# Optimization experiments

Hardware: AMD Instinct MI355X
Metric: run time of the kernel (lower is better)

## Reference

```python
import jax, jax.numpy as jnp
import numpy as np

B, N = 1, 512
CS, CZ, H, CH, PQ, PV = 384, 128, 12, 16, 4, 8
INF, EPS = 1e5, 1e-8
SOFTPLUS_INV_1 = 0.541324854612918


def _init_linear(key, fan_in, fan_out):
    kw, kb = jax.random.split(key)
    std = float(1.0 / np.sqrt(fan_in))
    w = jax.random.normal(kw, (fan_in, fan_out), dtype=jnp.float32) * std
    b = jnp.zeros((fan_out,), dtype=jnp.float32)
    return w, b


def setup_inputs() -> dict:
    key = jax.random.key(0)
    ks = jax.random.split(key, 12)
    s = jax.random.normal(ks[0], (B, N, CS), dtype=jnp.float32)
    z = jax.random.normal(ks[1], (B, N, N, CZ), dtype=jnp.float32) * 0.1
    # proper rotation matrices via QR of random Gaussians
    rot, _ = jnp.linalg.qr(jax.random.normal(ks[2], (B, N, 3, 3), dtype=jnp.float32))
    trans = jax.random.normal(ks[3], (B, N, 3), dtype=jnp.float32) * 10.0
    mask = jnp.ones((B, N), dtype=jnp.float32)
    w_q, b_q = _init_linear(ks[4], CS, H * CH)
    w_kv, b_kv = _init_linear(ks[5], CS, 2 * H * CH)
    w_qp, b_qp = _init_linear(ks[6], CS, H * PQ * 3)
    w_kvp, b_kvp = _init_linear(ks[7], CS, H * (PQ + PV) * 3)
    w_b, b_b = _init_linear(ks[8], CZ, H)
    head_weights = jnp.full((H,), SOFTPLUS_INV_1, dtype=jnp.float32)
    concat_dim = H * (CZ + CH + PV * 4)
    # 'final' init -> zeros
    w_out = jnp.zeros((concat_dim, CS), dtype=jnp.float32)
    b_out = jnp.zeros((CS,), dtype=jnp.float32)
    return dict(s=s, z=z, rot=rot, trans=trans, mask=mask,
                w_q=w_q, b_q=b_q, w_kv=w_kv, b_kv=b_kv,
                w_qp=w_qp, b_qp=b_qp, w_kvp=w_kvp, b_kvp=b_kvp,
                w_b=w_b, b_b=b_b, head_weights=head_weights,
                w_out=w_out, b_out=b_out)


def reference(s, z, rot, trans, mask,
              w_q, b_q, w_kv, b_kv, w_qp, b_qp, w_kvp, b_kvp,
              w_b, b_b, head_weights, w_out, b_out):
    # scalar q/k/v: [B,N,H,CH]
    q = (s @ w_q + b_q).reshape(B, N, H, CH)
    kv = (s @ w_kv + b_kv).reshape(B, N, H, 2 * CH)
    k, v = kv[..., :CH], kv[..., CH:]

    def make_points(w, b, P):
        p = s @ w + b                                   # [B,N,3*H*P] (x|y|z chunks)
        p = jnp.moveaxis(p.reshape(B, N, 3, H * P), -2, -1)  # [B,N,H*P,3]
        p = jnp.einsum('bnij,bnpj->bnpi', rot, p) + trans[:, :, None]  # global frame
        return p.reshape(B, N, H, P, 3)

    q_pts = make_points(w_qp, b_qp, PQ)                 # [B,N,H,PQ,3]
    kv_pts = make_points(w_kvp, b_kvp, PQ + PV)
    k_pts, v_pts = kv_pts[..., :PQ, :], kv_pts[..., PQ:, :]

    # scalar QK attention + pair bias
    a = jnp.einsum('bqhc,bkhc->bhqk', q, k) * float(np.sqrt(1.0 / (3 * CH)))
    b_bias = z @ w_b + b_b                              # [B,N,N,H]
    a = a + float(np.sqrt(1.0 / 3.0)) * jnp.moveaxis(b_bias, -1, -3)

    # squared point-distance attention
    d = q_pts[:, :, None] - k_pts[:, None]              # [B,N,N,H,PQ,3]
    pt_att = jnp.sum(d * d, axis=-1)                    # [B,N,N,H,PQ]
    hw = jax.nn.softplus(head_weights) * float(np.sqrt(1.0 / (3 * (PQ * 9.0 / 2))))
    pt_att = -0.5 * jnp.sum(pt_att * hw[None, None, None, :, None], axis=-1)  # [B,N,N,H]
    a = a + jnp.moveaxis(pt_att, -1, -3)                # [B,H,N,N]

    sq_mask = (mask[:, :, None] * mask[:, None, :] - 1.0) * INF
    a = jax.nn.softmax(a + sq_mask[:, None], axis=-1)   # [B,H,N,N]

    # standard value path
    o = jnp.einsum('bhqk,bkhc->bqhc', a, v).reshape(B, N, H * CH)
    # point value path, rotated back to local frame
    o_pt = jnp.einsum('bhqk,bkhpc->bqhpc', a, v_pts)    # [B,N,H,PV,3]
    o_pt = jnp.einsum('bnji,bnhpj->bnhpi', rot, o_pt - trans[:, :, None, None])
    o_pt_norm = jnp.sqrt(jnp.sum(o_pt ** 2, axis=-1) + EPS).reshape(B, N, H * PV)
    o_pt = o_pt.reshape(B, N, H * PV, 3)
    # pair-weighted path
    o_pair = jnp.einsum('bhqk,bqkc->bqhc', a, z).reshape(B, N, H * CZ)

    o_cat = jnp.concatenate(
        [o, o_pt[..., 0], o_pt[..., 1], o_pt[..., 2], o_pt_norm, o_pair], axis=-1)
    return o_cat @ w_out + b_out
```

## Files before the change

### kernel.cpp

```cpp
#include <hip/hip_runtime.h>
#include <math.h>

#define NRES 512
#define CSD  384
#define CZD  128

#define OFF_Q     0
#define OFF_KT    98304
#define OFF_VC    196608
#define OFF_QP    458752
#define OFF_KPT   532480
#define OFF_A     606208
#define OFF_OCAT  3751936
#define OFF_WCAT  4833280
#define OFF_BCAT  (OFF_WCAT + 442368)
#define OFF_PRAWQ 5276800
#define OFF_PRAWK 5350528
#define OFF_PART  OFF_A

__global__ __launch_bounds__(256) void k_wcat(
    const float* __restrict__ w_q, const float* __restrict__ b_q,
    const float* __restrict__ w_kv, const float* __restrict__ b_kv,
    const float* __restrict__ w_qp, const float* __restrict__ b_qp,
    const float* __restrict__ w_kvp, const float* __restrict__ b_kvp,
    float* __restrict__ wcat, float* __restrict__ bcat)
{
    const int idx = blockIdx.x * 256 + threadIdx.x;
    if (idx < 442368) {
        const int k = idx / 1152, c = idx % 1152;
        float v;
        if (c < 192)      v = w_q[k*192 + c];
        else if (c < 576) v = w_kv[k*384 + (c - 192)];
        else if (c < 720) v = w_qp[k*144 + (c - 576)];
        else              v = w_kvp[k*432 + (c - 720)];
        wcat[idx] = v;
    } else if (idx < 443520) {
        const int c = idx - 442368;
        float v;
        if (c < 192)      v = b_q[c];
        else if (c < 576) v = b_kv[c - 192];
        else if (c < 720) v = b_qp[c - 576];
        else              v = b_kvp[c - 720];
        bcat[c] = v;
    }
}

__global__ __launch_bounds__(256) void k_proj2(
    const float* __restrict__ s, const float* __restrict__ wcat, const float* __restrict__ bcat,
    float* __restrict__ q, float* __restrict__ kkT, float* __restrict__ vcomb,
    float* __restrict__ praw_q, float* __restrict__ praw_kv)
{
    const int ct = blockIdx.x;
    const int n0 = blockIdx.y * 32;
    const int t = threadIdx.x;

    __shared__ float sT[32][34];
    __shared__ float wt[32][36];

    const int lr = t >> 3, lc4 = t & 7;
    const int tr = t >> 4, tc = t & 15;
    float4 sv4, wv4;

    sv4 = *(const float4*)&s[(n0 + lr) * CSD + lc4 * 4];
    wv4 = *(const float4*)&wcat[lr * 1152 + ct * 32 + lc4 * 4];
    sT[lc4*4+0][lr] = sv4.x; sT[lc4*4+1][lr] = sv4.y; sT[lc4*4+2][lr] = sv4.z; sT[lc4*4+3][lr] = sv4.w;
    *(float4*)&wt[lr][lc4*4] = wv4;
    __syncthreads();

    float a00 = 0.f, a01 = 0.f, a10 = 0.f, a11 = 0.f;

    for (int it = 0; it < 12; ++it) {
        if (it < 11) {
            const int k0 = (it + 1) * 32;
            sv4 = *(const float4*)&s[(n0 + lr) * CSD + k0 + lc4 * 4];
            wv4 = *(const float4*)&wcat[(k0 + lr) * 1152 + ct * 32 + lc4 * 4];
        }
        #pragma unroll
        for (int kx = 0; kx < 32; ++kx) {
            float2 ss = *(const float2*)&sT[kx][tr * 2];
            float2 ww = *(const float2*)&wt[kx][tc * 2];
            a00 += ss.x * ww.x; a01 += ss.x * ww.y;
            a10 += ss.y * ww.x; a11 += ss.y * ww.y;
        }
        __syncthreads();
        if (it < 11) {
            sT[lc4*4+0][lr] = sv4.x; sT[lc4*4+1][lr] = sv4.y; sT[lc4*4+2][lr] = sv4.z; sT[lc4*4+3][lr] = sv4.w;
            *(float4*)&wt[lr][lc4*4] = wv4;
            __syncthreads();
        }
    }

    float accv[2][2] = {{a00, a01}, {a10, a11}};
    #pragma unroll
    for (int i = 0; i < 2; ++i) {
        const int n = n0 + tr * 2 + i;
        #pragma unroll
        for (int j = 0; j < 2; ++j) {
            const int gcol = ct * 32 + tc * 2 + j;
            const float v = accv[i][j] + bcat[gcol];
            if (gcol < 192) {
                q[n*192 + gcol] = v;
            } else if (gcol < 576) {
                int g = gcol - 192, h = g >> 5, cc = g & 31;
                if (cc < 16) kkT[(h*16 + cc)*NRES + n] = v;
                else         vcomb[n*NRES + h*16 + (cc-16)] = v;
            } else if (gcol < 720) {
                praw_q[n*144 + (gcol - 576)] = v;
            } else {
                praw_kv[n*432 + (gcol - 720)] = v;
            }
        }
    }
}

__global__ __launch_bounds__(256) void k_rot(
    const float* __restrict__ praw_q, const float* __restrict__ praw_kv,
    const float* __restrict__ rot, const float* __restrict__ trans,
    float* __restrict__ q_pts, float* __restrict__ kptsT, float* __restrict__ vcomb)
{
    const int idx = blockIdx.x * 256 + threadIdx.x;
    const int n = idx / 192, u = idx % 192;
    const float* R = rot + n*9;
    const float* T = trans + n*3;
    float px, py, pz;
    if (u < 48) {
        px = praw_q[n*144 + u]; py = praw_q[n*144 + 48 + u]; pz = praw_q[n*144 + 96 + u];
    } else {
        int pt = u - 48;
        px = praw_kv[n*432 + pt]; py = praw_kv[n*432 + 144 + pt]; pz = praw_kv[n*432 + 288 + pt];
    }
    float x  = R[0]*px + R[1]*py + R[2]*pz + T[0];
    float y  = R[3]*px + R[4]*py + R[5]*pz + T[1];
    float zc = R[6]*px + R[7]*py + R[8]*pz + T[2];
    if (u < 48) {
        int o = (n*48 + u)*3;
        q_pts[o] = x; q_pts[o+1] = y; q_pts[o+2] = zc;
    } else {
        int pt = u - 48;
        int h = pt / 12, pp = pt % 12;
        if (pp < 4) {
            int dim = (h*4 + pp)*3;
            kptsT[(dim+0)*NRES + n] = x;
            kptsT[(dim+1)*NRES + n] = y;
            kptsT[(dim+2)*NRES + n] = zc;
        } else {
            int u2 = (h*8 + (pp-4))*3;
            vcomb[n*NRES + 192 + u2+0] = x;
            vcomb[n*NRES + 192 + u2+1] = y;
            vcomb[n*NRES + 192 + u2+2] = zc;
        }
    }
}

__global__ __launch_bounds__(256) void k_bias3(
    const float* __restrict__ z, const float* __restrict__ w_b, const float* __restrict__ b_b,
    const float* __restrict__ q, const float* __restrict__ kkT,
    const float* __restrict__ q_pts, const float* __restrict__ kptsT,
    const float* __restrict__ head_weights, const float* __restrict__ mask,
    float* __restrict__ logitsT)
{
    const int k0 = blockIdx.x * 64;
    const int qn = blockIdx.y;
    const int t = threadIdx.x;
    __shared__ float zt[64*128];
    __shared__ float wbT[12*128];
    __shared__ float q_lds[192];
    __shared__ float qp_lds[144];
    __shared__ float hw_lds[12];

    const float4* zp4 = (const float4*)(z + ((size_t)qn*NRES + k0)*CZD);
    float4 zstg[8];
    #pragma unroll
    for (int r = 0; r < 8; ++r) zstg[r] = zp4[t + r*256];
    #pragma unroll
    for (int r = 0; r < 8; ++r) {
        const int idx = t + r*256;
        const int row = idx >> 5, c4 = idx & 31;
        const int sc4 = c4 ^ ((row & 7) << 2);
        *(float4*)&zt[row*128 + sc4*4] = zstg[r];
    }
    for (int i = t; i < 1536; i += 256) {
        const int h = i >> 7, c = i & 127;
        wbT[h*128 + c] = w_b[c*12 + h];
    }
    if (t < 192) q_lds[t] = q[qn*192 + t];
    if (t < 144) qp_lds[t] = q_pts[qn*144 + t];
    if (t < 12)  hw_lds[t] = logf(1.f + expf(head_weights[t])) * 0.13608276f;
    __syncthreads();

    const int k = t & 63;
    const int h0 = (t >> 6) * 3;
    float acc0 = 0.f, acc1 = 0.f, acc2 = 0.f;
    const float* zr = &zt[k*128];
    const float* w0 = &wbT[(h0+0)*128];
    const float* w1 = &wbT[(h0+1)*128];
    const float* w2 = &wbT[(h0+2)*128];
    const int sw = (k & 7) << 2;
    #pragma unroll
    for (int c4 = 0; c4 < 32; ++c4) {
        const int sc4 = c4 ^ sw;
        float4 zv  = *(const float4*)&zr[sc4*4];
        float4 wa  = *(const float4*)&w0[c4*4];
        float4 wbv = *(const float4*)&w1[c4*4];
        float4 wc  = *(const float4*)&w2[c4*4];
        acc0 += zv.x*wa.x  + zv.y*wa.y  + zv.z*wa.z  + zv.w*wa.w;
        acc1 += zv.x*wbv.x + zv.y*wbv.y + zv.z*wbv.z + zv.w*wbv.w;
        acc2 += zv.x*wc.x  + zv.y*wc.y  + zv.z*wc.z  + zv.w*wc.w;
    }

    const int kn = k0 + k;
    const float mterm = (mask[qn]*mask[kn] - 1.f) * 100000.f;
    float biasv[3] = {acc0 + b_b[h0+0], acc1 + b_b[h0+1], acc2 + b_b[h0+2]};
    #pragma unroll
    for (int j = 0; j < 3; ++j) {
        const int h = h0 + j;
        float qk = 0.f;
        const float* kT = kkT + (size_t)(h*16)*NRES + kn;
        #pragma unroll
        for (int c = 0; c < 16; ++c) qk += q_lds[h*16 + c] * kT[(size_t)c*NRES];
        float dsum = 0.f;
        const float* kpT = kptsT + (size_t)(h*12)*NRES + kn;
        #pragma unroll
        for (int d = 0; d < 12; ++d) { float df = qp_lds[h*12 + d] - kpT[(size_t)d*NRES]; dsum += df*df; }
        logitsT[(size_t)h*NRES*NRES + (size_t)qn*NRES + kn] =
            0.14433757f*qk + 0.57735027f*biasv[j] - 0.5f*hw_lds[h]*dsum + mterm;
    }
}

__global__ __launch_bounds__(256) void k_row5(
    const float* __restrict__ z, const float* __restrict__ logitsT,
    const float* __restrict__ vcomb,
    const float* __restrict__ rot, const float* __restrict__ trans,
    float* __restrict__ o_cat)
{
    const int qn = blockIdx.x;
    const int t = threadIdx.x;

    __shared__ float a_lds[12][521];
    __shared__ float pred[4][12][128];
    __shared__ float optraw[288];

    for (int i = t; i < 12*NRES; i += 256)
        a_lds[i >> 9][i & 511] = logitsT[(size_t)(i >> 9)*NRES*NRES + (size_t)qn*NRES + (i & 511)];
    __syncthreads();

    {
        const int w = t >> 6, lane = t & 63;
        for (int h = w; h < 12; h += 4) {
            float m = -1e30f;
            #pragma unroll
            for (int i = 0; i < 8; ++i) m = fmaxf(m, a_lds[h][lane + i*64]);
            #pragma unroll
            for (int off = 32; off > 0; off >>= 1) m = fmaxf(m, __shfl_xor(m, off));
            float ss = 0.f;
            #pragma unroll
            for (int i = 0; i < 8; ++i) {
                float e = __expf(a_lds[h][lane + i*64] - m);
                a_lds[h][lane + i*64] = e;
                ss += e;
            }
            #pragma unroll
            for (int off = 32; off > 0; off >>= 1) ss += __shfl_xor(ss, off);
            float inv = 1.f / ss;
            #pragma unroll
            for (int i = 0; i < 8; ++i) a_lds[h][lane + i*64] *= inv;
        }
    }
    __syncthreads();

    {
        const int c4 = t & 31, kgrp = t >> 5;
        const float4* zp = (const float4*)(z + (size_t)qn*NRES*CZD) + c4;
        float4 acc4[12];
        #pragma unroll
        for (int h = 0; h < 12; ++h) acc4[h] = make_float4(0.f,0.f,0.f,0.f);

        #pragma unroll 8
        for (int kn = kgrp; kn < NRES; kn += 8) {
            float4 zv = zp[kn*32];
            #pragma unroll
            for (int h = 0; h < 12; ++h) {
                float av = a_lds[h][kn];
                acc4[h].x += av*zv.x; acc4[h].y += av*zv.y;
                acc4[h].z += av*zv.z; acc4[h].w += av*zv.w;
            }
        }
        #pragma unroll
        for (int h = 0; h < 12; ++h) {
            acc4[h].x += __shfl_xor(acc4[h].x, 32);
            acc4[h].y += __shfl_xor(acc4[h].y, 32);
            acc4[h].z += __shfl_xor(acc4[h].z, 32);
            acc4[h].w += __shfl_xor(acc4[h].w, 32);
        }
        const int wave = t >> 6;
        if ((t & 63) < 32) {
            #pragma unroll
            for (int h = 0; h < 12; ++h) {
                pred[wave][h][c4*4+0] = acc4[h].x;
                pred[wave][h][c4*4+1] = acc4[h].y;
                pred[wave][h][c4*4+2] = acc4[h].z;
                pred[wave][h][c4*4+3] = acc4[h].w;
            }
        }
        __syncthreads();
        for (int i = t; i < 1536; i += 256) {
            int h = i >> 7, c = i & 127;
            float v = pred[0][h][c] + pred[1][h][c] + pred[2][h][c] + pred[3][h][c];
            o_cat[qn*2112 + 576 + h*128 + c] = v;
        }
    }

    if (t < 240) {
        const int ch0 = 2*t, ch1 = 2*t + 1;
        const int hA = (ch0 < 192) ? (ch0 >> 4) : (ch0 - 192) / 24;
        const int hB = (ch1 < 192) ? (ch1 >> 4) : (ch1 - 192) / 24;
        float aAcc = 0.f, bAcc = 0.f;
        const float2* vp2 = (const float2*)vcomb + t;
        #pragma unroll 8
        for (int kn = 0; kn < NRES; ++kn) {
            float2 v = vp2[(size_t)kn*256];
            aAcc += a_lds[hA][kn] * v.x;
            bAcc += a_lds[hB][kn] * v.y;
        }
        if (ch0 < 192) o_cat[qn*2112 + ch0] = aAcc;
        else           optraw[ch0 - 192] = aAcc;
        if (ch1 < 192) o_cat[qn*2112 + ch1] = bAcc;
        else           optraw[ch1 - 192] = bAcc;
    }
    __syncthreads();

    if (t < 96) {
        const float* R = rot + qn*9;
        const float* T = trans + qn*3;
        float ox = optraw[t*3]   - T[0];
        float oy = optraw[t*3+1] - T[1];
        float oz = optraw[t*3+2] - T[2];
        float x  = R[0]*ox + R[3]*oy + R[6]*oz;
        float y  = R[1]*ox + R[4]*oy + R[7]*oz;
        float zc = R[2]*ox + R[5]*oy + R[8]*oz;
        float* ob = o_cat + qn*2112;
        ob[192 + t] = x;
        ob[288 + t] = y;
        ob[384 + t] = zc;
        ob[480 + t] = sqrtf(x*x + y*y + zc*zc + 1e-8f);
    }
}

__global__ __launch_bounds__(256) void k_out2(
    const float* __restrict__ o_cat, const float* __restrict__ w_out, float* __restrict__ part)
{
    const int ct = blockIdx.x;
    const int n0 = blockIdx.y * 32;
    const int kc = blockIdx.z;
    const int t = threadIdx.x;

    __shared__ float oT[32][34];
    __shared__ float wt[32][36];

    const int lr = t >> 3, lc4 = t & 7;
    const int tr = t >> 4, tc = t & 15;
    const int kbase = kc * 352;
    float4 ov4, wv4;

    ov4 = *(const float4*)&o_cat[(n0 + lr) * 2112 + kbase + lc4 * 4];
    wv4 = *(const float4*)&w_out[(kbase + lr) * 384 + ct * 32 + lc4 * 4];
    oT[lc4*4+0][lr] = ov4.x; oT[lc4*4+1][lr] = ov4.y; oT[lc4*4+2][lr] = ov4.z; oT[lc4*4+3][lr] = ov4.w;
    *(float4*)&wt[lr][lc4*4] = wv4;
    __syncthreads();

    float a00 = 0.f, a01 = 0.f, a10 = 0.f, a11 = 0.f;

    for (int it = 0; it < 11; ++it) {
        if (it < 10) {
            const int k0 = kbase + (it + 1) * 32;
            ov4 = *(const float4*)&o_cat[(n0 + lr) * 2112 + k0 + lc4 * 4];
            wv4 = *(const float4*)&w_out[(k0 + lr) * 384 + ct * 32 + lc4 * 4];
        }
        #pragma unroll
        for (int kx = 0; kx < 32; ++kx) {
            float2 oo = *(const float2*)&oT[kx][tr * 2];
            float2 ww = *(const float2*)&wt[kx][tc * 2];
            a00 += oo.x * ww.x; a01 += oo.x * ww.y;
            a10 += oo.y * ww.x; a11 += oo.y * ww.y;
        }
        __syncthreads();
        if (it < 10) {
            oT[lc4*4+0][lr] = ov4.x; oT[lc4*4+1][lr] = ov4.y; oT[lc4*4+2][lr] = ov4.z; oT[lc4*4+3][lr] = ov4.w;
            *(float4*)&wt[lr][lc4*4] = wv4;
            __syncthreads();
        }
    }

    float* pp = part + (size_t)kc * 196608;
    pp[(n0 + tr*2 + 0)*384 + ct*32 + tc*2 + 0] = a00;
    pp[(n0 + tr*2 + 0)*384 + ct*32 + tc*2 + 1] = a01;
    pp[(n0 + tr*2 + 1)*384 + ct*32 + tc*2 + 0] = a10;
    pp[(n0 + tr*2 + 1)*384 + ct*32 + tc*2 + 1] = a11;
}

__global__ __launch_bounds__(256) void k_red(
    const float* __restrict__ part, const float* __restrict__ b_out, float* __restrict__ out)
{
    const int i = blockIdx.x*256 + threadIdx.x;
    float acc = b_out[i % 384];
    #pragma unroll
    for (int dc = 0; dc < 6; ++dc) acc += part[(size_t)dc*196608 + i];
    out[i] = acc;
}

extern "C" void kernel_launch(void* const* d_in, const int* in_sizes, int n_in,
                              void* d_out, int out_size, void* d_ws, size_t ws_size,
                              hipStream_t stream) {
    (void)in_sizes; (void)n_in; (void)out_size; (void)ws_size;
    const float* s      = (const float*)d_in[0];
    const float* z      = (const float*)d_in[1];
    const float* rot    = (const float*)d_in[2];
    const float* trans  = (const float*)d_in[3];
    const float* mask   = (const float*)d_in[4];
    const float* w_q    = (const float*)d_in[5];
    const float* b_q    = (const float*)d_in[6];
    const float* w_kv   = (const float*)d_in[7];
    const float* b_kv   = (const float*)d_in[8];
    const float* w_qp   = (const float*)d_in[9];
    const float* b_qp   = (const float*)d_in[10];
    const float* w_kvp  = (const float*)d_in[11];
    const float* b_kvp  = (const float*)d_in[12];
    const float* w_b    = (const float*)d_in[13];
    const float* b_b    = (const float*)d_in[14];
    const float* hwts   = (const float*)d_in[15];
    const float* w_out  = (const float*)d_in[16];
    const float* b_out  = (const float*)d_in[17];
    float* out = (float*)d_out;
    float* ws  = (float*)d_ws;

    float* q       = ws + OFF_Q;
    float* kkT     = ws + OFF_KT;
    float* vcomb   = ws + OFF_VC;
    float* qp      = ws + OFF_QP;
    float* kptsT   = ws + OFF_KPT;
    float* logitsT = ws + OFF_A;
    float* ocat    = ws + OFF_OCAT;
    float* wcat    = ws + OFF_WCAT;
    float* bcat    = ws + OFF_BCAT;
    float* part    = ws + OFF_PART;
    float* praw_q  = ws + OFF_PRAWQ;
    float* praw_kv = ws + OFF_PRAWK;

    k_wcat<<<dim3(1733), dim3(256), 0, stream>>>(w_q, b_q, w_kv, b_kv, w_qp, b_qp, w_kvp, b_kvp, wcat, bcat);
    k_proj2<<<dim3(36, 16), dim3(256), 0, stream>>>(s, wcat, bcat, q, kkT, vcomb, praw_q, praw_kv);
    k_rot<<<dim3(384), dim3(256), 0, stream>>>(praw_q, praw_kv, rot, trans, qp, kptsT, vcomb);
    k_bias3<<<dim3(8, NRES), dim3(256), 0, stream>>>(z, w_b, b_b, q, kkT, qp, kptsT,
        hwts, mask, logitsT);
    k_row5<<<dim3(NRES), dim3(256), 0, stream>>>(z, logitsT, vcomb, rot, trans, ocat);
    k_out2<<<dim3(12, 16, 6), dim3(256), 0, stream>>>(ocat, w_out, part);
    k_red<<<dim3(768), dim3(256), 0, stream>>>(part, b_out, out);
}
```

Before: 173.9 us.

## Precompute transposed pair-bias weights and restructure bias and row kernels' shared layouts

```diff
diff --git a/kernel.cpp b/kernel.cpp
--- a/kernel.cpp
+++ b/kernel.cpp
@@ -16,6 +16,7 @@
 #define OFF_BCAT  (OFF_WCAT + 442368)
 #define OFF_PRAWQ 5276800
 #define OFF_PRAWK 5350528
+#define OFF_WBT   5571712
 #define OFF_PART  OFF_A
 
 __global__ __launch_bounds__(256) void k_wcat(
@@ -23,7 +24,8 @@
     const float* __restrict__ w_kv, const float* __restrict__ b_kv,
     const float* __restrict__ w_qp, const float* __restrict__ b_qp,
     const float* __restrict__ w_kvp, const float* __restrict__ b_kvp,
-    float* __restrict__ wcat, float* __restrict__ bcat)
+    const float* __restrict__ w_b,
+    float* __restrict__ wcat, float* __restrict__ bcat, float* __restrict__ wbT)
 {
     const int idx = blockIdx.x * 256 + threadIdx.x;
     if (idx < 442368) {
@@ -42,6 +44,10 @@
         else if (c < 720) v = b_qp[c - 576];
         else              v = b_kvp[c - 720];
         bcat[c] = v;
+    } else if (idx < 445056) {
+        const int j = idx - 443520;
+        const int h = j >> 7, c = j & 127;
+        wbT[h*128 + c] = w_b[c*12 + h];
     }
 }
 
@@ -152,8 +158,8 @@
     }
 }
 
-__global__ __launch_bounds__(256) void k_bias3(
-    const float* __restrict__ z, const float* __restrict__ w_b, const float* __restrict__ b_b,
+__global__ __launch_bounds__(256) void k_bias4(
+    const float* __restrict__ z, const float* __restrict__ wbT, const float* __restrict__ b_b,
     const float* __restrict__ q, const float* __restrict__ kkT,
     const float* __restrict__ q_pts, const float* __restrict__ kptsT,
     const float* __restrict__ head_weights, const float* __restrict__ mask,
@@ -163,7 +169,7 @@
     const int qn = blockIdx.y;
     const int t = threadIdx.x;
     __shared__ float zt[64*128];
-    __shared__ float wbT[12*128];
+    __shared__ float part[4][64][13];
     __shared__ float q_lds[192];
     __shared__ float qp_lds[144];
     __shared__ float hw_lds[12];
@@ -176,58 +182,78 @@
     for (int r = 0; r < 8; ++r) {
         const int idx = t + r*256;
         const int row = idx >> 5, c4 = idx & 31;
-        const int sc4 = c4 ^ ((row & 7) << 2);
+        const int sc4 = c4 ^ (row & 7);
         *(float4*)&zt[row*128 + sc4*4] = zstg[r];
-    }
-    for (int i = t; i < 1536; i += 256) {
-        const int h = i >> 7, c = i & 127;
-        wbT[h*128 + c] = w_b[c*12 + h];
     }
     if (t < 192) q_lds[t] = q[qn*192 + t];
     if (t < 144) qp_lds[t] = q_pts[qn*144 + t];
     if (t < 12)  hw_lds[t] = logf(1.f + expf(head_weights[t])) * 0.13608276f;
     __syncthreads();
 
-    const int k = t & 63;
-    const int h0 = (t >> 6) * 3;
-    float acc0 = 0.f, acc1 = 0.f, acc2 = 0.f;
-    const float* zr = &zt[k*128];
-    const float* w0 = &wbT[(h0+0)*128];
-    const float* w1 = &wbT[(h0+1)*128];
-    const float* w2 = &wbT[(h0+2)*128];
-    const int sw = (k & 7) << 2;
-    #pragma unroll
-    for (int c4 = 0; c4 < 32; ++c4) {
-        const int sc4 = c4 ^ sw;
-        float4 zv  = *(const float4*)&zr[sc4*4];
-        float4 wa  = *(const float4*)&w0[c4*4];
-        float4 wbv = *(const float4*)&w1[c4*4];
-        float4 wc  = *(const float4*)&w2[c4*4];
-        acc0 += zv.x*wa.x  + zv.y*wa.y  + zv.z*wa.z  + zv.w*wa.w;
-        acc1 += zv.x*wbv.x + zv.y*wbv.y + zv.z*wbv.z + zv.w*wbv.w;
-        acc2 += zv.x*wc.x  + zv.y*wc.y  + zv.z*wc.z  + zv.w*wc.w;
-    }
-
-    const int kn = k0 + k;
-    const float mterm = (mask[qn]*mask[kn] - 1.f) * 100000.f;
-    float biasv[3] = {acc0 + b_b[h0+0], acc1 + b_b[h0+1], acc2 + b_b[h0+2]};
-    #pragma unroll
-    for (int j = 0; j < 3; ++j) {
-        const int h = h0 + j;
-        float qk = 0.f;
-        const float* kT = kkT + (size_t)(h*16)*NRES + kn;
-        #pragma unroll
-        for (int c = 0; c < 16; ++c) qk += q_lds[h*16 + c] * kT[(size_t)c*NRES];
-        float dsum = 0.f;
-        const float* kpT = kptsT + (size_t)(h*12)*NRES + kn;
-        #pragma unroll
-        for (int d = 0; d < 12; ++d) { float df = qp_lds[h*12 + d] - kpT[(size_t)d*NRES]; dsum += df*df; }
-        logitsT[(size_t)h*NRES*NRES + (size_t)qn*NRES + kn] =
-            0.14433757f*qk + 0.57735027f*biasv[j] - 0.5f*hw_lds[h]*dsum + mterm;
-    }
-}
-
-__global__ __launch_bounds__(256) void k_row5(
+    {
+        const int kgrp = t & 15, cgrp = (t >> 4) & 3, hgrp = t >> 6;
+        const int h0 = hgrp * 3;
+        const int kx7 = kgrp & 7;
+        const float* w0 = wbT + (h0+0)*128 + cgrp*32;
+        const float* w1 = wbT + (h0+1)*128 + cgrp*32;
+        const float* w2 = wbT + (h0+2)*128 + cgrp*32;
+        float acc[4][3];
+        #pragma unroll
+        for (int kk = 0; kk < 4; ++kk)
+            #pragma unroll
+            for (int j = 0; j < 3; ++j) acc[kk][j] = 0.f;
+        #pragma unroll
+        for (int j = 0; j < 8; ++j) {
+            const int c4 = cgrp*8 + j;
+            const float4 wa  = *(const float4*)&w0[j*4];
+            const float4 wbv = *(const float4*)&w1[j*4];
+            const float4 wc  = *(const float4*)&w2[j*4];
+            const int sc4 = c4 ^ kx7;
+            #pragma unroll
+            for (int kk = 0; kk < 4; ++kk) {
+                const int k = kgrp + 16*kk;
+                float4 zv = *(const float4*)&zt[k*128 + sc4*4];
+                acc[kk][0] += zv.x*wa.x  + zv.y*wa.y  + zv.z*wa.z  + zv.w*wa.w;
+                acc[kk][1] += zv.x*wbv.x + zv.y*wbv.y + zv.z*wbv.z + zv.w*wbv.w;
+                acc[kk][2] += zv.x*wc.x  + zv.y*wc.y  + zv.z*wc.z  + zv.w*wc.w;
+            }
+        }
+        #pragma unroll
+        for (int kk = 0; kk < 4; ++kk)
+            #pragma unroll
+            for (int j = 0; j < 3; ++j)
+                part[cgrp][kgrp + 16*kk][h0 + j] = acc[kk][j];
+    }
+    __syncthreads();
+
+    {
+        const int k = t & 63;
+        const int h0 = (t >> 6) * 3;
+        const int kn = k0 + k;
+        const float mterm = (mask[qn]*mask[kn] - 1.f) * 100000.f;
+        float biasv[3];
+        #pragma unroll
+        for (int j = 0; j < 3; ++j)
+            biasv[j] = b_b[h0+j] + part[0][k][h0+j] + part[1][k][h0+j]
+                     + part[2][k][h0+j] + part[3][k][h0+j];
+        #pragma unroll
+        for (int j = 0; j < 3; ++j) {
+            const int h = h0 + j;
+            float qk = 0.f;
+            const float* kT = kkT + (size_t)(h*16)*NRES + kn;
+            #pragma unroll
+            for (int c = 0; c < 16; ++c) qk += q_lds[h*16 + c] * kT[(size_t)c*NRES];
+            float dsum = 0.f;
+            const float* kpT = kptsT + (size_t)(h*12)*NRES + kn;
+            #pragma unroll
+            for (int d = 0; d < 12; ++d) { float df = qp_lds[h*12 + d] - kpT[(size_t)d*NRES]; dsum += df*df; }
+            logitsT[(size_t)h*NRES*NRES + (size_t)qn*NRES + kn] =
+                0.14433757f*qk + 0.57735027f*biasv[j] - 0.5f*hw_lds[h]*dsum + mterm;
+        }
+    }
+}
+
+__global__ __launch_bounds__(256) void k_row6(
     const float* __restrict__ z, const float* __restrict__ logitsT,
     const float* __restrict__ vcomb,
     const float* __restrict__ rot, const float* __restrict__ trans,
@@ -236,77 +262,77 @@
     const int qn = blockIdx.x;
     const int t = threadIdx.x;
 
-    __shared__ float a_lds[12][521];
-    __shared__ float pred[4][12][128];
+    __shared__ float aT[512*20];
     __shared__ float optraw[288];
 
-    for (int i = t; i < 12*NRES; i += 256)
-        a_lds[i >> 9][i & 511] = logitsT[(size_t)(i >> 9)*NRES*NRES + (size_t)qn*NRES + (i & 511)];
+    for (int i = t; i < 12*NRES; i += 256) {
+        const int h = i >> 9, kn = i & 511;
+        aT[kn*20 + h] = logitsT[(size_t)h*NRES*NRES + (size_t)qn*NRES + kn];
+    }
     __syncthreads();
 
     {
         const int w = t >> 6, lane = t & 63;
         for (int h = w; h < 12; h += 4) {
+            float v[8];
             float m = -1e30f;
             #pragma unroll
-            for (int i = 0; i < 8; ++i) m = fmaxf(m, a_lds[h][lane + i*64]);
+            for (int i = 0; i < 8; ++i) {
+                v[i] = aT[(lane + i*64)*20 + h];
+                m = fmaxf(m, v[i]);
+            }
             #pragma unroll
             for (int off = 32; off > 0; off >>= 1) m = fmaxf(m, __shfl_xor(m, off));
             float ss = 0.f;
             #pragma unroll
-            for (int i = 0; i < 8; ++i) {
-                float e = __expf(a_lds[h][lane + i*64] - m);
-                a_lds[h][lane + i*64] = e;
-                ss += e;
-            }
+            for (int i = 0; i < 8; ++i) { v[i] = __expf(v[i] - m); ss += v[i]; }
             #pragma unroll
             for (int off = 32; off > 0; off >>= 1) ss += __shfl_xor(ss, off);
-            float inv = 1.f / ss;
-            #pragma unroll
-            for (int i = 0; i < 8; ++i) a_lds[h][lane + i*64] *= inv;
+            const float inv = 1.f / ss;
+            #pragma unroll
+            for (int i = 0; i < 8; ++i) aT[(lane + i*64)*20 + h] = v[i] * inv;
         }
     }
     __syncthreads();
 
     {
-        const int c4 = t & 31, kgrp = t >> 5;
+        const int lane = t & 63, w = t >> 6;
+        const int c4 = w*8 + (lane & 7);
+        const int kg = lane >> 3;
         const float4* zp = (const float4*)(z + (size_t)qn*NRES*CZD) + c4;
         float4 acc4[12];
         #pragma unroll
         for (int h = 0; h < 12; ++h) acc4[h] = make_float4(0.f,0.f,0.f,0.f);
 
-        #pragma unroll 8
-        for (int kn = kgrp; kn < NRES; kn += 8) {
-            float4 zv = zp[kn*32];
+        #pragma unroll 4
+        for (int i = 0; i < 64; ++i) {
+            const int kn = kg + 8*i;
+            float4 zv = zp[(size_t)kn*32];
+            float4 a0 = *(const float4*)&aT[kn*20 + 0];
+            float4 a1 = *(const float4*)&aT[kn*20 + 4];
+            float4 a2 = *(const float4*)&aT[kn*20 + 8];
+            float av[12] = {a0.x,a0.y,a0.z,a0.w, a1.x,a1.y,a1.z,a1.w, a2.x,a2.y,a2.z,a2.w};
             #pragma unroll
             for (int h = 0; h < 12; ++h) {
-                float av = a_lds[h][kn];
-                acc4[h].x += av*zv.x; acc4[h].y += av*zv.y;
-                acc4[h].z += av*zv.z; acc4[h].w += av*zv.w;
+                acc4[h].x += av[h]*zv.x; acc4[h].y += av[h]*zv.y;
+                acc4[h].z += av[h]*zv.z; acc4[h].w += av[h]*zv.w;
             }
         }
         #pragma unroll
         for (int h = 0; h < 12; ++h) {
-            acc4[h].x += __shfl_xor(acc4[h].x, 32);
-            acc4[h].y += __shfl_xor(acc4[h].y, 32);
-            acc4[h].z += __shfl_xor(acc4[h].z, 32);
-            acc4[h].w += __shfl_xor(acc4[h].w, 32);
-        }
-        const int wave = t >> 6;
-        if ((t & 63) < 32) {
-            #pragma unroll
-            for (int h = 0; h < 12; ++h) {
-                pred[wave][h][c4*4+0] = acc4[h].x;
-                pred[wave][h][c4*4+1] = acc4[h].y;
-                pred[wave][h][c4*4+2] = acc4[h].z;
-                pred[wave][h][c4*4+3] = acc4[h].w;
+            #pragma unroll
+            for (int off = 8; off < 64; off <<= 1) {
+                acc4[h].x += __shfl_xor(acc4[h].x, off);
+                acc4[h].y += __shfl_xor(acc4[h].y, off);
+                acc4[h].z += __shfl_xor(acc4[h].z, off);
+                acc4[h].w += __shfl_xor(acc4[h].w, off);
             }
         }
-        __syncthreads();
-        for (int i = t; i < 1536; i += 256) {
-            int h = i >> 7, c = i & 127;
-            float v = pred[0][h][c] + pred[1][h][c] + pred[2][h][c] + pred[3][h][c];
-            o_cat[qn*2112 + 576 + h*128 + c] = v;
+        if (kg == 0) {
+            float* ob = o_cat + qn*2112 + 576;
+            #pragma unroll
+            for (int h = 0; h < 12; ++h)
+                *(float4*)&ob[h*128 + c4*4] = acc4[h];
         }
     }
 
@@ -319,8 +345,8 @@
         #pragma unroll 8
         for (int kn = 0; kn < NRES; ++kn) {
             float2 v = vp2[(size_t)kn*256];
-            aAcc += a_lds[hA][kn] * v.x;
-            bAcc += a_lds[hB][kn] * v.y;
+            aAcc += aT[kn*20 + hA] * v.x;
+            bAcc += aT[kn*20 + hB] * v.y;
         }
         if (ch0 < 192) o_cat[qn*2112 + ch0] = aAcc;
         else           optraw[ch0 - 192] = aAcc;
@@ -442,16 +468,18 @@
     float* ocat    = ws + OFF_OCAT;
     float* wcat    = ws + OFF_WCAT;
     float* bcat    = ws + OFF_BCAT;
+    float* wbT     = ws + OFF_WBT;
     float* part    = ws + OFF_PART;
     float* praw_q  = ws + OFF_PRAWQ;
     float* praw_kv = ws + OFF_PRAWK;
 
-    k_wcat<<<dim3(1733), dim3(256), 0, stream>>>(w_q, b_q, w_kv, b_kv, w_qp, b_qp, w_kvp, b_kvp, wcat, bcat);
+    k_wcat<<<dim3(1739), dim3(256), 0, stream>>>(w_q, b_q, w_kv, b_kv, w_qp, b_qp, w_kvp, b_kvp,
+        w_b, wcat, bcat, wbT);
     k_proj2<<<dim3(36, 16), dim3(256), 0, stream>>>(s, wcat, bcat, q, kkT, vcomb, praw_q, praw_kv);
     k_rot<<<dim3(384), dim3(256), 0, stream>>>(praw_q, praw_kv, rot, trans, qp, kptsT, vcomb);
-    k_bias3<<<dim3(8, NRES), dim3(256), 0, stream>>>(z, w_b, b_b, q, kkT, qp, kptsT,
+    k_bias4<<<dim3(8, NRES), dim3(256), 0, stream>>>(z, wbT, b_b, q, kkT, qp, kptsT,
         hwts, mask, logitsT);
-    k_row5<<<dim3(NRES), dim3(256), 0, stream>>>(z, logitsT, vcomb, rot, trans, ocat);
+    k_row6<<<dim3(NRES), dim3(256), 0, stream>>>(z, logitsT, vcomb, rot, trans, ocat);
     k_out2<<<dim3(12, 16, 6), dim3(256), 0, stream>>>(ocat, w_out, part);
     k_red<<<dim3(768), dim3(256), 0, stream>>>(part, b_out, out);
 }
```

Result: faster. 167.2 us (-3.9%).
